# Kernel tuning notes

Hardware: AMD Instinct MI355X
Metric: run time of the kernel (lower is better)

Reference implementation:

```python
import jax, jax.numpy as jnp
import numpy as np

B, N, D_IN, D_OUT = 16, 2048, 128, 128

def setup_inputs() -> dict:
    key = jax.random.key(0)
    ks = jax.random.split(key, 8)
    x = jax.random.normal(ks[0], (B, N, D_IN), dtype=jnp.float32)
    adj = jax.random.randint(ks[1], (N, N), 0, 2).astype(jnp.float32)
    # Conv1d(kernel_size=1) weights, PyTorch default uniform init scale
    s_emb = 1.0 / np.sqrt(D_IN)
    W_emb = jax.random.uniform(ks[2], (D_OUT, D_IN), jnp.float32, -s_emb, s_emb)
    b_emb = jax.random.uniform(ks[3], (D_OUT,), jnp.float32, -s_emb, s_emb)
    s_qk = 1.0 / np.sqrt(D_OUT)
    w_q = jax.random.uniform(ks[4], (D_OUT,), jnp.float32, -s_qk, s_qk)
    b_q = jax.random.uniform(ks[5], (1,), jnp.float32, -s_qk, s_qk)
    w_k = jax.random.uniform(ks[6], (D_OUT,), jnp.float32, -s_qk, s_qk)
    b_k = jax.random.uniform(ks[7], (1,), jnp.float32, -s_qk, s_qk)
    return {"x": x, "adj": adj, "W_emb": W_emb, "b_emb": b_emb,
            "w_q": w_q, "b_q": b_q, "w_k": w_k, "b_k": b_k}

def reference(x, adj, W_emb, b_emb, w_q, b_q, w_k, b_k):
    # emb_conv: 1x1 conv over node dim == per-node linear  [B,N,D_out]
    seq_fts = jnp.einsum('bni,oi->bno', x, W_emb) + b_emb
    # q_conv / k_conv: project to scalar per node  [B,N]
    q = jnp.einsum('bnd,d->bn', seq_fts, w_q) + b_q  # f_1_t squeezed
    k = jnp.einsum('bnd,d->bn', seq_fts, w_k) + b_k  # f_2_t squeezed
    # f[b,i,j] = f_1_t[b,0,j] + f_2_t^T[b,i,0] = q[b,j] + k[b,i]
    f = k[:, :, None] + q[:, None, :]                 # [B,N,N]
    f = jax.nn.leaky_relu(adj[None, :, :] * f, negative_slope=0.01)
    coefs = jax.nn.softmax(f, axis=1)                 # softmax over dim=1 (rows)
    vals = jnp.einsum('bij,bjd->bid', coefs, seq_fts)  # [B,N,D_out]
    return vals
```

## Files before the change

### kernel.cpp

```cpp
#include <hip/hip_runtime.h>
#include <hip/hip_bf16.h>
#include <stdint.h>

#define B_ 16
#define N_ 2048
#define D_ 128

typedef __bf16 bf16_t;
typedef bf16_t bf16x8 __attribute__((ext_vector_type(8)));
typedef float f32x4 __attribute__((ext_vector_type(4)));

__global__ __launch_bounds__(256) void k_pack_adj(const float* __restrict__ adj,
                                                  unsigned int* __restrict__ bits) {
    int t = blockIdx.x * 256 + threadIdx.x;
    float v = adj[t];
    unsigned long long m = __ballot(v > 0.5f);
    if ((t & 63) == 0) {
        int i = t >> 11;
        int j = t & 2047;
        bits[i * 64 + (j >> 5)]     = (unsigned int)m;
        bits[i * 64 + (j >> 5) + 1] = (unsigned int)(m >> 32);
    }
}

__global__ __launch_bounds__(256, 2) void k_emb(const float* __restrict__ x,
                                                const float* __restrict__ W,
                                                const float* __restrict__ be,
                                                const float* __restrict__ wq,
                                                const float* __restrict__ bq,
                                                const float* __restrict__ wk,
                                                const float* __restrict__ bk,
                                                bf16_t* __restrict__ Pb,
                                                float* __restrict__ qa, float* __restrict__ ka,
                                                float* __restrict__ Eq, float* __restrict__ eqs,
                                                float* __restrict__ Ek, float* __restrict__ eks) {
    __shared__ float xs[32][68];
    __shared__ float ws[32][132];
    __shared__ float qs[64], ks[64];
    int b  = blockIdx.y;
    int n0 = blockIdx.x * 64;
    int tid = threadIdx.x;
    int tx = tid & 15, ty = tid >> 4;
    if (tid < 64) { qs[tid] = 0.f; ks[tid] = 0.f; }

    float acc[4][8] = {};
    f32x4 xr[2], wr[4];

    auto loadregs = [&](int kc) {
#pragma unroll
        for (int s = 0; s < 2; ++s) {
            int p = tid + 256 * s;
            int n = p >> 3, kq = p & 7;
            xr[s] = *(const f32x4*)(x + ((size_t)(b * N_ + n0 + n)) * D_ + kc * 32 + kq * 4);
        }
#pragma unroll
        for (int s = 0; s < 4; ++s) {
            int p = tid + 256 * s;
            int d = p >> 3, kq = p & 7;
            wr[s] = *(const f32x4*)(W + (size_t)d * D_ + kc * 32 + kq * 4);
        }
    };
    auto writelds = [&]() {
#pragma unroll
        for (int s = 0; s < 2; ++s) {
            int p = tid + 256 * s;
            int n = p >> 3, kq = p & 7;
#pragma unroll
            for (int u = 0; u < 4; ++u) xs[kq * 4 + u][n] = xr[s][u];
        }
#pragma unroll
        for (int s = 0; s < 4; ++s) {
            int p = tid + 256 * s;
            int d = p >> 3, kq = p & 7;
#pragma unroll
            for (int u = 0; u < 4; ++u) ws[kq * 4 + u][d] = wr[s][u];
        }
    };

    loadregs(0);
    for (int kc = 0; kc < 4; ++kc) {
        writelds();
        __syncthreads();
        if (kc < 3) loadregs(kc + 1);
#pragma unroll 4
        for (int k = 0; k < 32; ++k) {
            f32x4 xv  = *(const f32x4*)&xs[k][tx * 4];
            f32x4 wv0 = *(const f32x4*)&ws[k][ty * 8];
            f32x4 wv1 = *(const f32x4*)&ws[k][ty * 8 + 4];
#pragma unroll
            for (int i = 0; i < 4; ++i)
#pragma unroll
                for (int j = 0; j < 8; ++j)
                    acc[i][j] += xv[i] * ((j < 4) ? wv0[j] : wv1[j - 4]);
        }
        __syncthreads();
    }

    float qp[4] = {}, kp[4] = {};
#pragma unroll
    for (int j = 0; j < 8; ++j) {
        int d = ty * 8 + j;
        float bj  = be[d];
        float wqj = wq[d];
        float wkj = wk[d];
        f32x4 o;
        bf16_t ob[4];
#pragma unroll
        for (int i = 0; i < 4; ++i) {
            o[i] = acc[i][j] + bj;
            qp[i] += o[i] * wqj;
            kp[i] += o[i] * wkj;
            ob[i] = (bf16_t)o[i];
        }
        *(uint2*)(Pb + ((size_t)b * D_ + d) * N_ + n0 + tx * 4) = *(uint2*)ob;
    }
#pragma unroll
    for (int i = 0; i < 4; ++i) {
        atomicAdd(&qs[tx * 4 + i], qp[i]);
        atomicAdd(&ks[tx * 4 + i], kp[i]);
    }
    __syncthreads();
    if (tid < 64) {
        int idx = b * N_ + n0 + tid;
        float aq = qs[tid] + bq[0];
        float ak = ks[tid] + bk[0];
        qa[idx] = aq;          ka[idx] = ak;
        Eq[idx] = expf(aq);    eqs[idx] = expf(0.01f * aq);
        Ek[idx] = expf(ak);    eks[idx] = expf(0.01f * ak);
    }
}

__global__ __launch_bounds__(256) void k_denom(const unsigned int* __restrict__ bits,
                                               const float* __restrict__ qa,
                                               const float* __restrict__ ka,
                                               const float* __restrict__ Eq,
                                               const float* __restrict__ eqs,
                                               const float* __restrict__ Ek,
                                               const float* __restrict__ eks,
                                               float* __restrict__ denom) {
    int jt  = blockIdx.x;
    int b   = blockIdx.y;
    int seg = blockIdx.z;
    int j = jt * 256 + threadIdx.x;
    float qj  = qa[b * N_ + j];
    float Eqj = Eq[b * N_ + j];
    float eqj = eqs[b * N_ + j];
    int shift = j & 31;
    int wid   = j >> 5;
    float acc = 0.f;
    int i0 = seg * 256;
#pragma unroll 16
    for (int i = i0; i < i0 + 256; ++i) {
        float kk  = ka[b * N_ + i];
        float Ekk = Ek[b * N_ + i];
        float ekk = eks[b * N_ + i];
        unsigned int w = bits[i * 64 + wid];
        float z  = kk + qj;
        float f1 = z > 0.f ? Ekk : ekk;
        float f2 = z > 0.f ? Eqj : eqj;
        float v  = f1 * f2;
        acc += ((w >> shift) & 1u) ? v : 1.0f;
    }
    atomicAdd(&denom[b * N_ + j], acc);
}

__global__ __launch_bounds__(256) void k_post(const float* __restrict__ denom,
                                              const float* __restrict__ Eq,
                                              const float* __restrict__ eqs,
                                              float* __restrict__ rd,
                                              float* __restrict__ Eqr,
                                              float* __restrict__ eqr) {
    int t = blockIdx.x * 256 + threadIdx.x;
    float r = 1.0f / denom[t];
    rd[t]  = r;
    Eqr[t] = Eq[t] * r;
    eqr[t] = eqs[t] * r;
}

__global__ __launch_bounds__(256, 2) void k_attn(const float* __restrict__ qa,
                                                 const float* __restrict__ ka,
                                                 const float* __restrict__ Ek,
                                                 const float* __restrict__ eks,
                                                 const float* __restrict__ rd,
                                                 const float* __restrict__ Eqr,
                                                 const float* __restrict__ eqr,
                                                 const unsigned int* __restrict__ bits,
                                                 const bf16_t* __restrict__ Pb,
                                                 float* __restrict__ out) {
    __shared__ __align__(16) bf16_t ldsB[2][128 * 64];
    __shared__ __align__(16) bf16_t ldsA[4 * 2 * 64 * 8];
    int b     = blockIdx.y;
    int ibase = blockIdx.x * 64;
    int tid   = threadIdx.x;
    int w     = tid >> 6;
    int lane  = tid & 63;
    int m16   = lane & 15;
    int quad  = lane >> 4;
    int ig    = w & 1;
    int dg    = w >> 1;

    int iA = ibase + (2 * ig) * 16 + m16;
    int iB = iA + 16;
    float mkR0 = -ka[b * N_ + iA], mkR1 = -ka[b * N_ + iB];
    float EkR0 = Ek[b * N_ + iA],  EkR1 = Ek[b * N_ + iB];
    float ekR0 = eks[b * N_ + iA], ekR1 = eks[b * N_ + iB];
    const unsigned int* brA = bits + (size_t)iA * 64;
    const unsigned int* brB = bits + (size_t)iB * 64;
    const float* qp  = qa  + b * N_;
    const float* Erp = Eqr + b * N_;
    const float* erp = eqr + b * N_;
    const float* rdp = rd  + b * N_;
    const bf16_t* PtB = Pb + (size_t)b * D_ * N_;

    f32x4 acc[2][4];
#pragma unroll
    for (int c = 0; c < 2; ++c)
#pragma unroll
        for (int nt = 0; nt < 4; ++nt) acc[c][nt] = (f32x4){0.f, 0.f, 0.f, 0.f};

    f32x4 qv4[2][2], Er4[2][2], er4[2][2], rd4[2][2];
    unsigned int mA[2], mB[2];

    auto ldj = [&](int par, int jb) {
        int j0 = jb + dg * 32 + quad * 8;
        qv4[par][0] = *(const f32x4*)(qp  + j0);
        qv4[par][1] = *(const f32x4*)(qp  + j0 + 4);
        Er4[par][0] = *(const f32x4*)(Erp + j0);
        Er4[par][1] = *(const f32x4*)(Erp + j0 + 4);
        er4[par][0] = *(const f32x4*)(erp + j0);
        er4[par][1] = *(const f32x4*)(erp + j0 + 4);
        rd4[par][0] = *(const f32x4*)(rdp + j0);
        rd4[par][1] = *(const f32x4*)(rdp + j0 + 4);
        mA[par] = brA[(jb >> 5) + dg];
        mB[par] = brB[(jb >> 5) + dg];
    };

    auto stage = [&](int bufi, int jb) {
#pragma unroll
        for (int t = 0; t < 4; ++t) {
            int off = t * 4096 + tid * 16;
            int d   = off >> 7;
            int g   = ((off & 127) >> 4) ^ (d & 7);
            const bf16_t* gp = PtB + (size_t)d * N_ + jb + g * 8;
            __builtin_amdgcn_global_load_lds(
                (const __attribute__((address_space(1))) void*)gp,
                (__attribute__((address_space(3))) void*)((char*)(&ldsB[bufi][0]) + off),
                16, 0, 0);
        }
    };

    stage(0, 0);
    ldj(0, 0);
    __syncthreads();
    int buf = 0;
#pragma unroll 1
    for (int s2 = 0; s2 < N_ / 128; ++s2) {
#pragma unroll
        for (int par = 0; par < 2; ++par) {
            int step = s2 * 2 + par;
            int jb = step * 64;
            if (step + 1 < N_ / 64) {
                ldj(par ^ 1, jb + 64);
                stage(buf ^ 1, jb + 64);
            }

            bf16x8 afA, afB;
#pragma unroll
            for (int t = 0; t < 8; ++t) {
                float qv = (t < 4) ? qv4[par][0][t] : qv4[par][1][t - 4];
                float Er = (t < 4) ? Er4[par][0][t] : Er4[par][1][t - 4];
                float er = (t < 4) ? er4[par][0][t] : er4[par][1][t - 4];
                float rj = (t < 4) ? rd4[par][0][t] : rd4[par][1][t - 4];
                int bit = quad * 8 + t;
                {
                    bool c = qv > mkR0;
                    float v = (c ? EkR0 : ekR0) * (c ? Er : er);
                    afA[t] = (bf16_t)(((mA[par] >> bit) & 1u) ? v : rj);
                }
                {
                    bool c = qv > mkR1;
                    float v = (c ? EkR1 : ekR1) * (c ? Er : er);
                    afB[t] = (bf16_t)(((mB[par] >> bit) & 1u) ? v : rj);
                }
            }
            *(bf16x8*)((char*)ldsA + ((((2 * ig + 0) * 2 + dg) * 64 + lane) * 16)) = afA;
            *(bf16x8*)((char*)ldsA + ((((2 * ig + 1) * 2 + dg) * 64 + lane) * 16)) = afB;

            asm volatile("s_waitcnt lgkmcnt(0)\n\ts_barrier" ::: "memory");

            {
                int cph = ((dg * 4 + quad) ^ (m16 & 7)) * 8;
#pragma unroll
                for (int nt = 0; nt < 4; ++nt) {
                    int d = dg * 64 + nt * 16 + m16;
                    bf16x8 bf = *(const bf16x8*)&ldsB[buf][d * 64 + cph];
                    acc[0][nt] = __builtin_amdgcn_mfma_f32_16x16x32_bf16(afA, bf, acc[0][nt], 0, 0, 0);
                    acc[1][nt] = __builtin_amdgcn_mfma_f32_16x16x32_bf16(afB, bf, acc[1][nt], 0, 0, 0);
                }
            }
            {
                int oh = 1 - dg;
                bf16x8 a0 = *(const bf16x8*)((char*)ldsA + ((((2 * ig + 0) * 2 + oh) * 64 + lane) * 16));
                bf16x8 a1 = *(const bf16x8*)((char*)ldsA + ((((2 * ig + 1) * 2 + oh) * 64 + lane) * 16));
                int cph = ((oh * 4 + quad) ^ (m16 & 7)) * 8;
#pragma unroll
                for (int nt = 0; nt < 4; ++nt) {
                    int d = dg * 64 + nt * 16 + m16;
                    bf16x8 bf = *(const bf16x8*)&ldsB[buf][d * 64 + cph];
                    acc[0][nt] = __builtin_amdgcn_mfma_f32_16x16x32_bf16(a0, bf, acc[0][nt], 0, 0, 0);
                    acc[1][nt] = __builtin_amdgcn_mfma_f32_16x16x32_bf16(a1, bf, acc[1][nt], 0, 0, 0);
                }
            }
            __syncthreads();
            buf ^= 1;
        }
    }

#pragma unroll
    for (int c = 0; c < 2; ++c) {
        int irow = ibase + (2 * ig + c) * 16 + quad * 4;
#pragma unroll
        for (int nt = 0; nt < 4; ++nt) {
            int d = dg * 64 + nt * 16 + m16;
#pragma unroll
            for (int r = 0; r < 4; ++r)
                out[((size_t)b * N_ + irow + r) * D_ + d] = acc[c][nt][r];
        }
    }
}

extern "C" void kernel_launch(void* const* d_in, const int* in_sizes, int n_in,
                              void* d_out, int out_size, void* d_ws, size_t ws_size,
                              hipStream_t stream) {
    const float* x   = (const float*)d_in[0];
    const float* adj = (const float*)d_in[1];
    const float* W   = (const float*)d_in[2];
    const float* be  = (const float*)d_in[3];
    const float* wq  = (const float*)d_in[4];
    const float* bq  = (const float*)d_in[5];
    const float* wk  = (const float*)d_in[6];
    const float* bk  = (const float*)d_in[7];
    float* out = (float*)d_out;

    char* ws = (char*)d_ws;
    size_t off = 0;
    bf16_t* Pb = (bf16_t*)(ws + off); off += (size_t)B_ * D_ * N_ * 2;
    float* qa  = (float*)(ws + off);  off += (size_t)B_ * N_ * 4;
    float* ka  = (float*)(ws + off);  off += (size_t)B_ * N_ * 4;
    float* denom = (float*)(ws + off); off += (size_t)B_ * N_ * 4;
    float* Eq  = (float*)(ws + off);  off += (size_t)B_ * N_ * 4;
    float* eqs = (float*)(ws + off);  off += (size_t)B_ * N_ * 4;
    float* Ek  = (float*)(ws + off);  off += (size_t)B_ * N_ * 4;
    float* eks = (float*)(ws + off);  off += (size_t)B_ * N_ * 4;
    float* rd  = (float*)(ws + off);  off += (size_t)B_ * N_ * 4;
    float* Eqr = (float*)(ws + off);  off += (size_t)B_ * N_ * 4;
    float* eqr = (float*)(ws + off);  off += (size_t)B_ * N_ * 4;
    unsigned int* bits = (unsigned int*)(ws + off); off += (size_t)N_ * 64 * 4;

    hipMemsetAsync(denom, 0, (size_t)B_ * N_ * 4, stream);

    k_pack_adj<<<N_ * N_ / 256, 256, 0, stream>>>(adj, bits);
    k_emb<<<dim3(N_ / 64, B_), 256, 0, stream>>>(x, W, be, wq, bq, wk, bk,
                                                 Pb, qa, ka, Eq, eqs, Ek, eks);
    k_denom<<<dim3(8, 16, 8), 256, 0, stream>>>(bits, qa, ka, Eq, eqs, Ek, eks, denom);
    k_post<<<B_ * N_ / 256, 256, 0, stream>>>(denom, Eq, eqs, rd, Eqr, eqr);
    k_attn<<<dim3(N_ / 64, B_), 256, 0, stream>>>(qa, ka, Ek, eks, rd, Eqr, eqr,
                                                  bits, Pb, out);
}
```

Measured before the change: 187.1 us.

## Fuse adjacency packing and denom zeroing into emb, post into denom, register-stage B

Packs the adjacency bitmask and zeroes denom and the new counters inside k_emb, which removes the memset and pack_adj launches. k_post is folded into k_denom through a last-block counter that computes the reciprocals. k_attn drops LDS staging of P: it loads B fragments straight into registers and software-pipelines A generation one step ahead with double-buffered LDS A. The cost is more register pressure in k_attn and global loads that are less coalesced.

After: 390.6 us. 109% more time.

```diff
diff --git a/kernel.cpp b/kernel.cpp
--- a/kernel.cpp
+++ b/kernel.cpp
@@ -10,21 +10,9 @@
 typedef bf16_t bf16x8 __attribute__((ext_vector_type(8)));
 typedef float f32x4 __attribute__((ext_vector_type(4)));
 
-__global__ __launch_bounds__(256) void k_pack_adj(const float* __restrict__ adj,
-                                                  unsigned int* __restrict__ bits) {
-    int t = blockIdx.x * 256 + threadIdx.x;
-    float v = adj[t];
-    unsigned long long m = __ballot(v > 0.5f);
-    if ((t & 63) == 0) {
-        int i = t >> 11;
-        int j = t & 2047;
-        bits[i * 64 + (j >> 5)]     = (unsigned int)m;
-        bits[i * 64 + (j >> 5) + 1] = (unsigned int)(m >> 32);
-    }
-}
-
 __global__ __launch_bounds__(256, 2) void k_emb(const float* __restrict__ x,
                                                 const float* __restrict__ W,
+                                                const float* __restrict__ adj,
                                                 const float* __restrict__ be,
                                                 const float* __restrict__ wq,
                                                 const float* __restrict__ bq,
@@ -33,12 +21,16 @@
                                                 bf16_t* __restrict__ Pb,
                                                 float* __restrict__ qa, float* __restrict__ ka,
                                                 float* __restrict__ Eq, float* __restrict__ eqs,
-                                                float* __restrict__ Ek, float* __restrict__ eks) {
+                                                float* __restrict__ Ek, float* __restrict__ eks,
+                                                unsigned int* __restrict__ bits,
+                                                float* __restrict__ denom,
+                                                int* __restrict__ counters) {
     __shared__ float xs[32][68];
     __shared__ float ws[32][132];
     __shared__ float qs[64], ks[64];
     int b  = blockIdx.y;
     int n0 = blockIdx.x * 64;
+    int flat = b * 32 + blockIdx.x;
     int tid = threadIdx.x;
     int tx = tid & 15, ty = tid >> 4;
     if (tid < 64) { qs[tid] = 0.f; ks[tid] = 0.f; }
@@ -78,6 +70,24 @@
     };
 
     loadregs(0);
+
+    {
+        int prow  = flat * 4 + (tid >> 6);
+        int pword = tid & 63;
+        const float* ap = adj + (size_t)prow * N_ + pword * 32;
+        unsigned int m = 0;
+#pragma unroll
+        for (int g = 0; g < 8; ++g) {
+            f32x4 v = *(const f32x4*)(ap + g * 4);
+#pragma unroll
+            for (int u = 0; u < 4; ++u)
+                m |= (v[u] > 0.5f ? 1u : 0u) << (g * 4 + u);
+        }
+        bits[prow * 64 + pword] = m;
+    }
+    if (tid < 64) denom[flat * 64 + tid] = 0.f;
+    if (tid == 64 && flat < 128) counters[flat] = 0;
+
     for (int kc = 0; kc < 4; ++kc) {
         writelds();
         __syncthreads();
@@ -137,7 +147,12 @@
                                                const float* __restrict__ eqs,
                                                const float* __restrict__ Ek,
                                                const float* __restrict__ eks,
-                                               float* __restrict__ denom) {
+                                               float* __restrict__ denom,
+                                               int* __restrict__ counters,
+                                               float* __restrict__ rd,
+                                               float* __restrict__ Eqr,
+                                               float* __restrict__ eqr) {
+    __shared__ int lastFlag;
     int jt  = blockIdx.x;
     int b   = blockIdx.y;
     int seg = blockIdx.z;
@@ -162,19 +177,21 @@
         acc += ((w >> shift) & 1u) ? v : 1.0f;
     }
     atomicAdd(&denom[b * N_ + j], acc);
-}
-
-__global__ __launch_bounds__(256) void k_post(const float* __restrict__ denom,
-                                              const float* __restrict__ Eq,
-                                              const float* __restrict__ eqs,
-                                              float* __restrict__ rd,
-                                              float* __restrict__ Eqr,
-                                              float* __restrict__ eqr) {
-    int t = blockIdx.x * 256 + threadIdx.x;
-    float r = 1.0f / denom[t];
-    rd[t]  = r;
-    Eqr[t] = Eq[t] * r;
-    eqr[t] = eqs[t] * r;
+    __threadfence();
+    if (threadIdx.x == 0) {
+        int old = atomicAdd(&counters[b * 8 + jt], 1);
+        lastFlag = (old == 7);
+    }
+    __syncthreads();
+    if (lastFlag) {
+        __threadfence();
+        int idx = b * N_ + j;
+        float dn = atomicAdd(&denom[idx], 0.0f);
+        float r = 1.0f / dn;
+        rd[idx]  = r;
+        Eqr[idx] = Eqj * r;
+        eqr[idx] = eqj * r;
+    }
 }
 
 __global__ __launch_bounds__(256, 2) void k_attn(const float* __restrict__ qa,
@@ -187,8 +204,7 @@
                                                  const unsigned int* __restrict__ bits,
                                                  const bf16_t* __restrict__ Pb,
                                                  float* __restrict__ out) {
-    __shared__ __align__(16) bf16_t ldsB[2][128 * 64];
-    __shared__ __align__(16) bf16_t ldsA[4 * 2 * 64 * 8];
+    __shared__ __align__(16) bf16_t ldsA[2 * 4 * 2 * 64 * 8];
     int b     = blockIdx.y;
     int ibase = blockIdx.x * 64;
     int tid   = threadIdx.x;
@@ -199,17 +215,17 @@
     int ig    = w & 1;
     int dg    = w >> 1;
 
-    int iA = ibase + (2 * ig) * 16 + m16;
+    int iA = ibase + 2 * ig * 16 + m16;
     int iB = iA + 16;
-    float mkR0 = -ka[b * N_ + iA], mkR1 = -ka[b * N_ + iB];
-    float EkR0 = Ek[b * N_ + iA],  EkR1 = Ek[b * N_ + iB];
-    float ekR0 = eks[b * N_ + iA], ekR1 = eks[b * N_ + iB];
+    float mk0 = -ka[b * N_ + iA], mk1 = -ka[b * N_ + iB];
+    float Ek0 = Ek[b * N_ + iA],  Ek1 = Ek[b * N_ + iB];
+    float ek0 = eks[b * N_ + iA], ek1 = eks[b * N_ + iB];
     const unsigned int* brA = bits + (size_t)iA * 64;
     const unsigned int* brB = bits + (size_t)iB * 64;
-    const float* qp  = qa  + b * N_;
-    const float* Erp = Eqr + b * N_;
-    const float* erp = eqr + b * N_;
-    const float* rdp = rd  + b * N_;
+    const float* qp = qa  + b * N_;
+    const float* Ep = Eqr + b * N_;
+    const float* ep = eqr + b * N_;
+    const float* rp = rd  + b * N_;
     const bf16_t* PtB = Pb + (size_t)b * D_ * N_;
 
     f32x4 acc[2][4];
@@ -218,101 +234,87 @@
 #pragma unroll
         for (int nt = 0; nt < 4; ++nt) acc[c][nt] = (f32x4){0.f, 0.f, 0.f, 0.f};
 
-    f32x4 qv4[2][2], Er4[2][2], er4[2][2], rd4[2][2];
+    f32x4 jq[2][2], jE[2][2], je[2][2], jr[2][2];
     unsigned int mA[2], mB[2];
-
-    auto ldj = [&](int par, int jb) {
+    bf16x8 Bv[2][8];
+    bf16x8 aOwn[2][2];
+
+    auto AOFF = [&](int par, int chunk, int hh, int ln) {
+        return (((par * 4 + chunk) * 2 + hh) * 64 + ln) * 16;
+    };
+
+    auto ldj = [&](int sl, int jb) {
         int j0 = jb + dg * 32 + quad * 8;
-        qv4[par][0] = *(const f32x4*)(qp  + j0);
-        qv4[par][1] = *(const f32x4*)(qp  + j0 + 4);
-        Er4[par][0] = *(const f32x4*)(Erp + j0);
-        Er4[par][1] = *(const f32x4*)(Erp + j0 + 4);
-        er4[par][0] = *(const f32x4*)(erp + j0);
-        er4[par][1] = *(const f32x4*)(erp + j0 + 4);
-        rd4[par][0] = *(const f32x4*)(rdp + j0);
-        rd4[par][1] = *(const f32x4*)(rdp + j0 + 4);
-        mA[par] = brA[(jb >> 5) + dg];
-        mB[par] = brB[(jb >> 5) + dg];
-    };
-
-    auto stage = [&](int bufi, int jb) {
-#pragma unroll
-        for (int t = 0; t < 4; ++t) {
-            int off = t * 4096 + tid * 16;
-            int d   = off >> 7;
-            int g   = ((off & 127) >> 4) ^ (d & 7);
-            const bf16_t* gp = PtB + (size_t)d * N_ + jb + g * 8;
-            __builtin_amdgcn_global_load_lds(
-                (const __attribute__((address_space(1))) void*)gp,
-                (__attribute__((address_space(3))) void*)((char*)(&ldsB[bufi][0]) + off),
-                16, 0, 0);
-        }
-    };
-
-    stage(0, 0);
+        jq[sl][0] = *(const f32x4*)(qp + j0);  jq[sl][1] = *(const f32x4*)(qp + j0 + 4);
+        jE[sl][0] = *(const f32x4*)(Ep + j0);  jE[sl][1] = *(const f32x4*)(Ep + j0 + 4);
+        je[sl][0] = *(const f32x4*)(ep + j0);  je[sl][1] = *(const f32x4*)(ep + j0 + 4);
+        jr[sl][0] = *(const f32x4*)(rp + j0);  jr[sl][1] = *(const f32x4*)(rp + j0 + 4);
+        mA[sl] = brA[(jb >> 5) + dg];
+        mB[sl] = brB[(jb >> 5) + dg];
+    };
+
+    auto ldB = [&](int sl, int jb) {
+#pragma unroll
+        for (int h2 = 0; h2 < 2; ++h2)
+#pragma unroll
+            for (int nt = 0; nt < 4; ++nt)
+                Bv[sl][h2 * 4 + nt] = *(const bf16x8*)(
+                    PtB + (size_t)(dg * 64 + nt * 16 + m16) * N_ + jb + h2 * 32 + quad * 8);
+    };
+
+    auto genA = [&](int src, int dst) {
+        bf16x8 fA, fB;
+#pragma unroll
+        for (int t = 0; t < 8; ++t) {
+            float qv = (t < 4) ? jq[src][0][t] : jq[src][1][t - 4];
+            float Er = (t < 4) ? jE[src][0][t] : jE[src][1][t - 4];
+            float er = (t < 4) ? je[src][0][t] : je[src][1][t - 4];
+            float rj = (t < 4) ? jr[src][0][t] : jr[src][1][t - 4];
+            int bit = quad * 8 + t;
+            {
+                bool c = qv > mk0;
+                float v = (c ? Ek0 : ek0) * (c ? Er : er);
+                fA[t] = (bf16_t)(((mA[src] >> bit) & 1u) ? v : rj);
+            }
+            {
+                bool c = qv > mk1;
+                float v = (c ? Ek1 : ek1) * (c ? Er : er);
+                fB[t] = (bf16_t)(((mB[src] >> bit) & 1u) ? v : rj);
+            }
+        }
+        aOwn[dst][0] = fA;
+        aOwn[dst][1] = fB;
+        *(bf16x8*)((char*)ldsA + AOFF(dst, 2 * ig + 0, dg, lane)) = fA;
+        *(bf16x8*)((char*)ldsA + AOFF(dst, 2 * ig + 1, dg, lane)) = fB;
+    };
+
     ldj(0, 0);
+    ldj(1, 64);
+    ldB(1, 0);
+    genA(0, 1);
     __syncthreads();
-    int buf = 0;
+
 #pragma unroll 1
     for (int s2 = 0; s2 < N_ / 128; ++s2) {
 #pragma unroll
         for (int par = 0; par < 2; ++par) {
             int step = s2 * 2 + par;
-            int jb = step * 64;
-            if (step + 1 < N_ / 64) {
-                ldj(par ^ 1, jb + 64);
-                stage(buf ^ 1, jb + 64);
+            if (step <= 29) ldj(par, (step + 2) * 64);
+            if (step <= 30) ldB(par, (step + 1) * 64);
+            if (step <= 30) genA(par ^ 1, par);
+
+            int src = par ^ 1;
+            bf16x8 o0 = *(const bf16x8*)((char*)ldsA + AOFF(src, 2 * ig + 0, 1 - dg, lane));
+            bf16x8 o1 = *(const bf16x8*)((char*)ldsA + AOFF(src, 2 * ig + 1, 1 - dg, lane));
+#pragma unroll
+            for (int nt = 0; nt < 4; ++nt) {
+                acc[0][nt] = __builtin_amdgcn_mfma_f32_16x16x32_bf16(aOwn[src][0], Bv[src][dg * 4 + nt], acc[0][nt], 0, 0, 0);
+                acc[1][nt] = __builtin_amdgcn_mfma_f32_16x16x32_bf16(aOwn[src][1], Bv[src][dg * 4 + nt], acc[1][nt], 0, 0, 0);
+                acc[0][nt] = __builtin_amdgcn_mfma_f32_16x16x32_bf16(o0, Bv[src][(1 - dg) * 4 + nt], acc[0][nt], 0, 0, 0);
+                acc[1][nt] = __builtin_amdgcn_mfma_f32_16x16x32_bf16(o1, Bv[src][(1 - dg) * 4 + nt], acc[1][nt], 0, 0, 0);
             }
-
-            bf16x8 afA, afB;
-#pragma unroll
-            for (int t = 0; t < 8; ++t) {
-                float qv = (t < 4) ? qv4[par][0][t] : qv4[par][1][t - 4];
-                float Er = (t < 4) ? Er4[par][0][t] : Er4[par][1][t - 4];
-                float er = (t < 4) ? er4[par][0][t] : er4[par][1][t - 4];
-                float rj = (t < 4) ? rd4[par][0][t] : rd4[par][1][t - 4];
-                int bit = quad * 8 + t;
-                {
-                    bool c = qv > mkR0;
-                    float v = (c ? EkR0 : ekR0) * (c ? Er : er);
-                    afA[t] = (bf16_t)(((mA[par] >> bit) & 1u) ? v : rj);
-                }
-                {
-                    bool c = qv > mkR1;
-                    float v = (c ? EkR1 : ekR1) * (c ? Er : er);
-                    afB[t] = (bf16_t)(((mB[par] >> bit) & 1u) ? v : rj);
-                }
-            }
-            *(bf16x8*)((char*)ldsA + ((((2 * ig + 0) * 2 + dg) * 64 + lane) * 16)) = afA;
-            *(bf16x8*)((char*)ldsA + ((((2 * ig + 1) * 2 + dg) * 64 + lane) * 16)) = afB;
-
-            asm volatile("s_waitcnt lgkmcnt(0)\n\ts_barrier" ::: "memory");
-
-            {
-                int cph = ((dg * 4 + quad) ^ (m16 & 7)) * 8;
-#pragma unroll
-                for (int nt = 0; nt < 4; ++nt) {
-                    int d = dg * 64 + nt * 16 + m16;
-                    bf16x8 bf = *(const bf16x8*)&ldsB[buf][d * 64 + cph];
-                    acc[0][nt] = __builtin_amdgcn_mfma_f32_16x16x32_bf16(afA, bf, acc[0][nt], 0, 0, 0);
-                    acc[1][nt] = __builtin_amdgcn_mfma_f32_16x16x32_bf16(afB, bf, acc[1][nt], 0, 0, 0);
-                }
-            }
-            {
-                int oh = 1 - dg;
-                bf16x8 a0 = *(const bf16x8*)((char*)ldsA + ((((2 * ig + 0) * 2 + oh) * 64 + lane) * 16));
-                bf16x8 a1 = *(const bf16x8*)((char*)ldsA + ((((2 * ig + 1) * 2 + oh) * 64 + lane) * 16));
-                int cph = ((oh * 4 + quad) ^ (m16 & 7)) * 8;
-#pragma unroll
-                for (int nt = 0; nt < 4; ++nt) {
-                    int d = dg * 64 + nt * 16 + m16;
-                    bf16x8 bf = *(const bf16x8*)&ldsB[buf][d * 64 + cph];
-                    acc[0][nt] = __builtin_amdgcn_mfma_f32_16x16x32_bf16(a0, bf, acc[0][nt], 0, 0, 0);
-                    acc[1][nt] = __builtin_amdgcn_mfma_f32_16x16x32_bf16(a1, bf, acc[1][nt], 0, 0, 0);
-                }
-            }
-            __syncthreads();
-            buf ^= 1;
+            if (step <= 30)
+                asm volatile("s_waitcnt lgkmcnt(0)\n\ts_barrier" ::: "memory");
         }
     }
 
@@ -356,14 +358,13 @@
     float* Eqr = (float*)(ws + off);  off += (size_t)B_ * N_ * 4;
     float* eqr = (float*)(ws + off);  off += (size_t)B_ * N_ * 4;
     unsigned int* bits = (unsigned int*)(ws + off); off += (size_t)N_ * 64 * 4;
-
-    hipMemsetAsync(denom, 0, (size_t)B_ * N_ * 4, stream);
-
-    k_pack_adj<<<N_ * N_ / 256, 256, 0, stream>>>(adj, bits);
-    k_emb<<<dim3(N_ / 64, B_), 256, 0, stream>>>(x, W, be, wq, bq, wk, bk,
-                                                 Pb, qa, ka, Eq, eqs, Ek, eks);
-    k_denom<<<dim3(8, 16, 8), 256, 0, stream>>>(bits, qa, ka, Eq, eqs, Ek, eks, denom);
-    k_post<<<B_ * N_ / 256, 256, 0, stream>>>(denom, Eq, eqs, rd, Eqr, eqr);
+    int* counters = (int*)(ws + off); off += 128 * 4;
+
+    k_emb<<<dim3(N_ / 64, B_), 256, 0, stream>>>(x, W, adj, be, wq, bq, wk, bk,
+                                                 Pb, qa, ka, Eq, eqs, Ek, eks,
+                                                 bits, denom, counters);
+    k_denom<<<dim3(8, 16, 8), 256, 0, stream>>>(bits, qa, ka, Eq, eqs, Ek, eks,
+                                                denom, counters, rd, Eqr, eqr);
     k_attn<<<dim3(N_ / 64, B_), 256, 0, stream>>>(qa, ka, Ek, eks, rd, Eqr, eqr,
                                                   bits, Pb, out);
 }
```

## Fuse adjacency packing and denom zeroing into emb kernel; halve attn row tile

Applied to the files above, without the earlier changes.

Adjacency bit-packing and zeroing of the softmax denominator move into k_emb, which drops a separate kernel and a memset launch. k_attn now handles 32 rows per block instead of 64, with one A fragment per wave and occupancy raised to 4 blocks. The q>-k comparison is rewritten as Er > rcp(Ek)*rd so qa and ka no longer need to be loaded. Smaller row tiles double how often each Pb tile is reloaded, and the reformulated comparison may differ near ties or for nonpositive Ek.

Result: slower. 200.3 us (+7.0%).

```diff
diff --git a/kernel.cpp b/kernel.cpp
--- a/kernel.cpp
+++ b/kernel.cpp
@@ -10,21 +10,9 @@
 typedef bf16_t bf16x8 __attribute__((ext_vector_type(8)));
 typedef float f32x4 __attribute__((ext_vector_type(4)));
 
-__global__ __launch_bounds__(256) void k_pack_adj(const float* __restrict__ adj,
-                                                  unsigned int* __restrict__ bits) {
-    int t = blockIdx.x * 256 + threadIdx.x;
-    float v = adj[t];
-    unsigned long long m = __ballot(v > 0.5f);
-    if ((t & 63) == 0) {
-        int i = t >> 11;
-        int j = t & 2047;
-        bits[i * 64 + (j >> 5)]     = (unsigned int)m;
-        bits[i * 64 + (j >> 5) + 1] = (unsigned int)(m >> 32);
-    }
-}
-
 __global__ __launch_bounds__(256, 2) void k_emb(const float* __restrict__ x,
                                                 const float* __restrict__ W,
+                                                const float* __restrict__ adj,
                                                 const float* __restrict__ be,
                                                 const float* __restrict__ wq,
                                                 const float* __restrict__ bq,
@@ -33,12 +21,15 @@
                                                 bf16_t* __restrict__ Pb,
                                                 float* __restrict__ qa, float* __restrict__ ka,
                                                 float* __restrict__ Eq, float* __restrict__ eqs,
-                                                float* __restrict__ Ek, float* __restrict__ eks) {
+                                                float* __restrict__ Ek, float* __restrict__ eks,
+                                                unsigned int* __restrict__ bits,
+                                                float* __restrict__ denom) {
     __shared__ float xs[32][68];
     __shared__ float ws[32][132];
     __shared__ float qs[64], ks[64];
     int b  = blockIdx.y;
     int n0 = blockIdx.x * 64;
+    int flat = b * 32 + blockIdx.x;
     int tid = threadIdx.x;
     int tx = tid & 15, ty = tid >> 4;
     if (tid < 64) { qs[tid] = 0.f; ks[tid] = 0.f; }
@@ -78,6 +69,23 @@
     };
 
     loadregs(0);
+
+    {
+        int prow  = flat * 4 + (tid >> 6);
+        int pword = tid & 63;
+        const float* ap = adj + (size_t)prow * N_ + pword * 32;
+        unsigned int m = 0;
+#pragma unroll
+        for (int g = 0; g < 8; ++g) {
+            f32x4 v = *(const f32x4*)(ap + g * 4);
+#pragma unroll
+            for (int u = 0; u < 4; ++u)
+                m |= (v[u] > 0.5f ? 1u : 0u) << (g * 4 + u);
+        }
+        bits[prow * 64 + pword] = m;
+    }
+    if (tid < 64) denom[flat * 64 + tid] = 0.f;
+
     for (int kc = 0; kc < 4; ++kc) {
         writelds();
         __syncthreads();
@@ -177,9 +185,7 @@
     eqr[t] = eqs[t] * r;
 }
 
-__global__ __launch_bounds__(256, 2) void k_attn(const float* __restrict__ qa,
-                                                 const float* __restrict__ ka,
-                                                 const float* __restrict__ Ek,
+__global__ __launch_bounds__(256, 4) void k_attn(const float* __restrict__ Ek,
                                                  const float* __restrict__ eks,
                                                  const float* __restrict__ rd,
                                                  const float* __restrict__ Eqr,
@@ -188,9 +194,9 @@
                                                  const bf16_t* __restrict__ Pb,
                                                  float* __restrict__ out) {
     __shared__ __align__(16) bf16_t ldsB[2][128 * 64];
-    __shared__ __align__(16) bf16_t ldsA[4 * 2 * 64 * 8];
+    __shared__ __align__(16) bf16_t ldsA[2 * 2 * 64 * 8];
     int b     = blockIdx.y;
-    int ibase = blockIdx.x * 64;
+    int ibase = blockIdx.x * 32;
     int tid   = threadIdx.x;
     int w     = tid >> 6;
     int lane  = tid & 63;
@@ -199,40 +205,29 @@
     int ig    = w & 1;
     int dg    = w >> 1;
 
-    int iA = ibase + (2 * ig) * 16 + m16;
-    int iB = iA + 16;
-    float mkR0 = -ka[b * N_ + iA], mkR1 = -ka[b * N_ + iB];
-    float EkR0 = Ek[b * N_ + iA],  EkR1 = Ek[b * N_ + iB];
-    float ekR0 = eks[b * N_ + iA], ekR1 = eks[b * N_ + iB];
-    const unsigned int* brA = bits + (size_t)iA * 64;
-    const unsigned int* brB = bits + (size_t)iB * 64;
-    const float* qp  = qa  + b * N_;
-    const float* Erp = Eqr + b * N_;
-    const float* erp = eqr + b * N_;
-    const float* rdp = rd  + b * N_;
+    int iR = ibase + ig * 16 + m16;
+    float EkR = Ek[b * N_ + iR];
+    float ekR = eks[b * N_ + iR];
+    float TR  = __builtin_amdgcn_rcpf(EkR);
+    const unsigned int* br = bits + (size_t)iR * 64;
+    const float* Ep = Eqr + b * N_;
+    const float* ep = eqr + b * N_;
+    const float* rp = rd  + b * N_;
     const bf16_t* PtB = Pb + (size_t)b * D_ * N_;
 
-    f32x4 acc[2][4];
-#pragma unroll
-    for (int c = 0; c < 2; ++c)
-#pragma unroll
-        for (int nt = 0; nt < 4; ++nt) acc[c][nt] = (f32x4){0.f, 0.f, 0.f, 0.f};
-
-    f32x4 qv4[2][2], Er4[2][2], er4[2][2], rd4[2][2];
-    unsigned int mA[2], mB[2];
-
-    auto ldj = [&](int par, int jb) {
+    f32x4 acc[4];
+#pragma unroll
+    for (int nt = 0; nt < 4; ++nt) acc[nt] = (f32x4){0.f, 0.f, 0.f, 0.f};
+
+    f32x4 jE[2][2], je[2][2], jr[2][2];
+    unsigned int msk[2];
+
+    auto ldj = [&](int sl, int jb) {
         int j0 = jb + dg * 32 + quad * 8;
-        qv4[par][0] = *(const f32x4*)(qp  + j0);
-        qv4[par][1] = *(const f32x4*)(qp  + j0 + 4);
-        Er4[par][0] = *(const f32x4*)(Erp + j0);
-        Er4[par][1] = *(const f32x4*)(Erp + j0 + 4);
-        er4[par][0] = *(const f32x4*)(erp + j0);
-        er4[par][1] = *(const f32x4*)(erp + j0 + 4);
-        rd4[par][0] = *(const f32x4*)(rdp + j0);
-        rd4[par][1] = *(const f32x4*)(rdp + j0 + 4);
-        mA[par] = brA[(jb >> 5) + dg];
-        mB[par] = brB[(jb >> 5) + dg];
+        jE[sl][0] = *(const f32x4*)(Ep + j0);  jE[sl][1] = *(const f32x4*)(Ep + j0 + 4);
+        je[sl][0] = *(const f32x4*)(ep + j0);  je[sl][1] = *(const f32x4*)(ep + j0 + 4);
+        jr[sl][0] = *(const f32x4*)(rp + j0);  jr[sl][1] = *(const f32x4*)(rp + j0 + 4);
+        msk[sl] = br[(jb >> 5) + dg];
     };
 
     auto stage = [&](int bufi, int jb) {
@@ -264,27 +259,17 @@
                 stage(buf ^ 1, jb + 64);
             }
 
-            bf16x8 afA, afB;
+            bf16x8 af;
 #pragma unroll
             for (int t = 0; t < 8; ++t) {
-                float qv = (t < 4) ? qv4[par][0][t] : qv4[par][1][t - 4];
-                float Er = (t < 4) ? Er4[par][0][t] : Er4[par][1][t - 4];
-                float er = (t < 4) ? er4[par][0][t] : er4[par][1][t - 4];
-                float rj = (t < 4) ? rd4[par][0][t] : rd4[par][1][t - 4];
-                int bit = quad * 8 + t;
-                {
-                    bool c = qv > mkR0;
-                    float v = (c ? EkR0 : ekR0) * (c ? Er : er);
-                    afA[t] = (bf16_t)(((mA[par] >> bit) & 1u) ? v : rj);
-                }
-                {
-                    bool c = qv > mkR1;
-                    float v = (c ? EkR1 : ekR1) * (c ? Er : er);
-                    afB[t] = (bf16_t)(((mB[par] >> bit) & 1u) ? v : rj);
-                }
+                float Er = (t < 4) ? jE[par][0][t] : jE[par][1][t - 4];
+                float er = (t < 4) ? je[par][0][t] : je[par][1][t - 4];
+                float rj = (t < 4) ? jr[par][0][t] : jr[par][1][t - 4];
+                bool c = Er > TR * rj;
+                float v = (c ? EkR : ekR) * (c ? Er : er);
+                af[t] = (bf16_t)(((msk[par] >> (quad * 8 + t)) & 1u) ? v : rj);
             }
-            *(bf16x8*)((char*)ldsA + ((((2 * ig + 0) * 2 + dg) * 64 + lane) * 16)) = afA;
-            *(bf16x8*)((char*)ldsA + ((((2 * ig + 1) * 2 + dg) * 64 + lane) * 16)) = afB;
+            *(bf16x8*)((char*)ldsA + (((ig * 2 + dg) * 64 + lane) * 16)) = af;
 
             asm volatile("s_waitcnt lgkmcnt(0)\n\ts_barrier" ::: "memory");
 
@@ -294,21 +279,18 @@
                 for (int nt = 0; nt < 4; ++nt) {
                     int d = dg * 64 + nt * 16 + m16;
                     bf16x8 bf = *(const bf16x8*)&ldsB[buf][d * 64 + cph];
-                    acc[0][nt] = __builtin_amdgcn_mfma_f32_16x16x32_bf16(afA, bf, acc[0][nt], 0, 0, 0);
-                    acc[1][nt] = __builtin_amdgcn_mfma_f32_16x16x32_bf16(afB, bf, acc[1][nt], 0, 0, 0);
+                    acc[nt] = __builtin_amdgcn_mfma_f32_16x16x32_bf16(af, bf, acc[nt], 0, 0, 0);
                 }
             }
             {
                 int oh = 1 - dg;
-                bf16x8 a0 = *(const bf16x8*)((char*)ldsA + ((((2 * ig + 0) * 2 + oh) * 64 + lane) * 16));
-                bf16x8 a1 = *(const bf16x8*)((char*)ldsA + ((((2 * ig + 1) * 2 + oh) * 64 + lane) * 16));
+                bf16x8 ao = *(const bf16x8*)((char*)ldsA + (((ig * 2 + oh) * 64 + lane) * 16));
                 int cph = ((oh * 4 + quad) ^ (m16 & 7)) * 8;
 #pragma unroll
                 for (int nt = 0; nt < 4; ++nt) {
                     int d = dg * 64 + nt * 16 + m16;
                     bf16x8 bf = *(const bf16x8*)&ldsB[buf][d * 64 + cph];
-                    acc[0][nt] = __builtin_amdgcn_mfma_f32_16x16x32_bf16(a0, bf, acc[0][nt], 0, 0, 0);
-                    acc[1][nt] = __builtin_amdgcn_mfma_f32_16x16x32_bf16(a1, bf, acc[1][nt], 0, 0, 0);
+                    acc[nt] = __builtin_amdgcn_mfma_f32_16x16x32_bf16(ao, bf, acc[nt], 0, 0, 0);
                 }
             }
             __syncthreads();
@@ -316,16 +298,13 @@
         }
     }
 
-#pragma unroll
-    for (int c = 0; c < 2; ++c) {
-        int irow = ibase + (2 * ig + c) * 16 + quad * 4;
-#pragma unroll
-        for (int nt = 0; nt < 4; ++nt) {
-            int d = dg * 64 + nt * 16 + m16;
-#pragma unroll
-            for (int r = 0; r < 4; ++r)
-                out[((size_t)b * N_ + irow + r) * D_ + d] = acc[c][nt][r];
-        }
+    int irow = ibase + ig * 16 + quad * 4;
+#pragma unroll
+    for (int nt = 0; nt < 4; ++nt) {
+        int d = dg * 64 + nt * 16 + m16;
+#pragma unroll
+        for (int r = 0; r < 4; ++r)
+            out[((size_t)b * N_ + irow + r) * D_ + d] = acc[nt][r];
     }
 }
 
@@ -357,13 +336,10 @@
     float* eqr = (float*)(ws + off);  off += (size_t)B_ * N_ * 4;
     unsigned int* bits = (unsigned int*)(ws + off); off += (size_t)N_ * 64 * 4;
 
-    hipMemsetAsync(denom, 0, (size_t)B_ * N_ * 4, stream);
-
-    k_pack_adj<<<N_ * N_ / 256, 256, 0, stream>>>(adj, bits);
-    k_emb<<<dim3(N_ / 64, B_), 256, 0, stream>>>(x, W, be, wq, bq, wk, bk,
-                                                 Pb, qa, ka, Eq, eqs, Ek, eks);
+    k_emb<<<dim3(N_ / 64, B_), 256, 0, stream>>>(x, W, adj, be, wq, bq, wk, bk,
+                                                 Pb, qa, ka, Eq, eqs, Ek, eks,
+                                                 bits, denom);
     k_denom<<<dim3(8, 16, 8), 256, 0, stream>>>(bits, qa, ka, Eq, eqs, Ek, eks, denom);
     k_post<<<B_ * N_ / 256, 256, 0, stream>>>(denom, Eq, eqs, rd, Eqr, eqr);
-    k_attn<<<dim3(N_ / 64, B_), 256, 0, stream>>>(qa, ka, Ek, eks, rd, Eqr, eqr,
-                                                  bits, Pb, out);
-}
+    k_attn<<<dim3(N_ / 32, B_), 256, 0, stream>>>(Ek, eks, rd, Eqr, eqr, bits, Pb, out);
+}
```
